# Optimization experiments

Hardware: AMD Instinct MI355X
Metric: run time of the kernel (lower is better)

The kernel has to match this reference:

```python
import jax, jax.numpy as jnp
import numpy as np

DIM = 96
D_STATE = 16
D_CONV = 3
D_INNER = 192   # int(DIM * 2.0)
DT_RANK = 6     # ceil(DIM / 16)
K = 4           # cross-scan directions
BATCH, H, W = 2, 56, 56


def setup_inputs() -> dict:
    key = jax.random.key(0)
    k = jax.random.split(key, 8)
    x = jax.random.normal(k[0], (BATCH, DIM, H, W), jnp.float32)
    W_in = jax.random.normal(k[1], (DIM, 2 * D_INNER), jnp.float32) / np.sqrt(DIM)
    W_conv = jax.random.normal(k[2], (D_INNER, 1, D_CONV, D_CONV), jnp.float32) / D_CONV
    b_conv = jnp.zeros((D_INNER,), jnp.float32)
    W_xproj = jax.random.normal(k[3], (K, D_INNER, DT_RANK + 2 * D_STATE), jnp.float32) / np.sqrt(D_INNER)
    W_dt = jax.random.normal(k[4], (K, DT_RANK, D_INNER), jnp.float32) / np.sqrt(DT_RANK)
    # dt bias init as in torch: dt ~ exp(U * (log 0.1 - log 0.001) + log 0.001), inv-softplus
    dt = jnp.exp(jax.random.uniform(k[5], (K, D_INNER), jnp.float32)
                 * (np.log(0.1) - np.log(0.001)) + np.log(0.001))
    dt = jnp.clip(dt, 1e-4, None)
    b_dt = dt + jnp.log(-jnp.expm1(-dt))
    A_logs = jnp.log(jnp.broadcast_to(jnp.arange(1, D_STATE + 1, dtype=jnp.float32),
                                      (K, D_INNER, D_STATE)))
    Ds = jnp.ones((K, D_INNER), jnp.float32)
    W_out = jax.random.normal(k[6], (D_INNER, DIM), jnp.float32) / np.sqrt(D_INNER)
    return dict(x=x, W_in=W_in, W_conv=W_conv, b_conv=b_conv, W_xproj=W_xproj,
                W_dt=W_dt, b_dt=b_dt, A_logs=A_logs, Ds=Ds, W_out=W_out)


def _ss2d(x, W_in, W_conv, b_conv, W_xproj, W_dt, b_dt, A_logs, Ds, W_out):
    Bsz, C, Hh, Ww = x.shape
    L = Hh * Ww
    # in_proj
    xf = x.transpose(0, 2, 3, 1).reshape(Bsz, L, C)        # (B, L, C)
    xz = xf @ W_in
    xp, z = jnp.split(xz, 2, axis=-1)                       # each (B, L, D)
    # depthwise conv + silu
    xi = xp.reshape(Bsz, Hh, Ww, -1).transpose(0, 3, 1, 2)  # (B, D, H, W)
    pad = D_CONV // 2
    xi = jax.lax.conv_general_dilated(
        xi, W_conv, (1, 1), ((pad, pad), (pad, pad)),
        feature_group_count=xi.shape[1],
        dimension_numbers=('NCHW', 'OIHW', 'NCHW')) + b_conv[None, :, None, None]
    xi = jax.nn.silu(xi)
    D = xi.shape[1]
    # cross-scan: 4 directions, each (B, L, D)
    x1 = xi.reshape(Bsz, D, L).transpose(0, 2, 1)
    x2 = xi[:, :, :, ::-1].reshape(Bsz, D, L).transpose(0, 2, 1)
    xt = xi.transpose(0, 1, 3, 2)                           # (B, D, W, H)
    x3 = xt.reshape(Bsz, D, L).transpose(0, 2, 1)
    x4 = xt[:, :, :, ::-1].reshape(Bsz, D, L).transpose(0, 2, 1)
    xs = jnp.stack([x1, x2, x3, x4])                        # (K, B, L, D)
    # per-direction projections, batched over K
    xdbl = jnp.einsum('kbld,kde->kble', xs, W_xproj)
    dr = xdbl[..., :DT_RANK]
    Bk = xdbl[..., DT_RANK:DT_RANK + D_STATE]               # (K, B, L, N)
    Ck = xdbl[..., DT_RANK + D_STATE:]                      # (K, B, L, N)
    delta = jax.nn.softplus(jnp.einsum('kblr,krd->kbld', dr, W_dt)
                            + b_dt[:, None, None, :])       # (K, B, L, D)
    A = -jnp.exp(A_logs)                                    # (K, D, N)

    def step(h, inp):
        x_i, d_i, B_i, C_i = inp  # (K,B,D), (K,B,D), (K,B,N), (K,B,N)
        dA = jnp.exp(d_i[..., None] * A[:, None])           # (K, B, D, N)
        h = dA * h + (d_i * x_i)[..., None] * B_i[:, :, None, :]
        y = jnp.einsum('kbdn,kbn->kbd', h, C_i)
        return h, y

    h0 = jnp.zeros((K, Bsz, D, D_STATE), xs.dtype)
    seq = (xs.transpose(2, 0, 1, 3), delta.transpose(2, 0, 1, 3),
           Bk.transpose(2, 0, 1, 3), Ck.transpose(2, 0, 1, 3))
    _, ys = jax.lax.scan(step, h0, seq)                     # (L, K, B, D)
    ys = ys.transpose(1, 2, 0, 3) + xs * Ds[:, None, None, :]  # (K, B, L, D)
    # cross-merge back to row-major (h w) order
    y1 = ys[0]
    y2 = ys[1].reshape(Bsz, Hh, Ww, D)[:, :, ::-1, :].reshape(Bsz, L, D)
    y3 = ys[2].reshape(Bsz, Ww, Hh, D).transpose(0, 2, 1, 3).reshape(Bsz, L, D)
    y4 = ys[3].reshape(Bsz, Ww, Hh, D)[:, :, ::-1, :].transpose(0, 2, 1, 3).reshape(Bsz, L, D)
    y = (y1 + y2 + y3 + y4) * jax.nn.silu(z)
    out = (y @ W_out).reshape(Bsz, Hh, Ww, C).transpose(0, 3, 1, 2)
    return out


def reference(x, W_in, W_conv, b_conv, W_xproj, W_dt, b_dt, A_logs, Ds, W_out):
    return _ss2d(x, W_in, W_conv, b_conv, W_xproj, W_dt, b_dt, A_logs, Ds, W_out)
```

## Files before the change

kernel.cpp:

```cpp
#include <hip/hip_runtime.h>
#include <math.h>

constexpr int BATCH  = 2;
constexpr int CDIM   = 96;
constexpr int HH     = 56;
constexpr int WW     = 56;
constexpr int LL     = HH * WW;
constexpr int DIN    = 192;
constexpr int NK     = 4;
constexpr int NST    = 16;
constexpr int RNK    = 6;
constexpr int EPROJ  = RNK + 2 * NST;
constexpr int SCH    = 64;
constexpr int NCH    = LL / SCH;
constexpr int CGRP   = DIN / 16;
constexpr int C_DPB  = 32;
constexpr int C_NBLK = DIN / C_DPB;

constexpr int STDU = SCH + 2;
constexpr int STB1 = SCH + 4;

constexpr size_t SZ_PX   = (size_t)BATCH * LL * DIN;
constexpr size_t OFF_XP  = 0;
constexpr size_t OFF_Z   = OFF_XP + SZ_PX;
constexpr size_t OFF_XI  = OFF_Z  + SZ_PX;
constexpr size_t OFF_DR  = OFF_XI + SZ_PX;
constexpr size_t SZ_DR   = (size_t)NK * BATCH * LL * 8;
constexpr size_t OFF_B   = OFF_DR + SZ_DR;
constexpr size_t SZ_BC   = (size_t)NK * BATCH * LL * NST;
constexpr size_t OFF_C   = OFF_B + SZ_BC;
constexpr size_t OFF_YD  = OFF_C + SZ_BC;
constexpr size_t SZ_YD   = (size_t)NK * BATCH * LL * DIN;
constexpr size_t OFF_HE  = OFF_YD + SZ_YD;
constexpr size_t SZ_HS   = (size_t)NK * BATCH * NCH * DIN * NST;
constexpr size_t OFF_WT  = OFF_HE + 2 * SZ_HS;
constexpr size_t SZ_WT   = (size_t)NK * EPROJ * DIN;

__device__ __forceinline__ float silu(float v) {
    return v / (1.0f + __expf(-v));
}

__device__ __forceinline__ float softplus_f(float x) {
    return (x > 20.0f) ? x : __logf(1.0f + __expf(x));
}

__device__ __forceinline__ int seq_to_lr(int k, int l) {
    int q = l / WW;
    int r = l - q * WW;
    if (k == 0) return l;
    if (k == 1) return q * WW + (WW - 1 - r);
    if (k == 2) return r * WW + q;
    return (WW - 1 - r) * WW + q;
}

__device__ __forceinline__ int spatial_to_seq(int k, int s) {
    int h = s / WW;
    int w = s - h * WW;
    if (k == 0) return s;
    if (k == 1) return h * WW + (WW - 1 - w);
    if (k == 2) return w * WW + h;
    return w * WW + (WW - 1 - h);
}

__device__ __forceinline__ size_t hs_idx(int c, int kb, int d, int n) {
    return ((size_t)(c * (NK * BATCH) + kb) * DIN + d) * NST + n;
}

__device__ __forceinline__ float4 delta4(
        float4 r03, float2 r45, const float4* wr, float4 bb4) {
    float4 raw = bb4;
    raw.x = fmaf(r03.x, wr[0].x, raw.x); raw.y = fmaf(r03.x, wr[0].y, raw.y);
    raw.z = fmaf(r03.x, wr[0].z, raw.z); raw.w = fmaf(r03.x, wr[0].w, raw.w);
    raw.x = fmaf(r03.y, wr[1].x, raw.x); raw.y = fmaf(r03.y, wr[1].y, raw.y);
    raw.z = fmaf(r03.y, wr[1].z, raw.z); raw.w = fmaf(r03.y, wr[1].w, raw.w);
    raw.x = fmaf(r03.z, wr[2].x, raw.x); raw.y = fmaf(r03.z, wr[2].y, raw.y);
    raw.z = fmaf(r03.z, wr[2].z, raw.z); raw.w = fmaf(r03.z, wr[2].w, raw.w);
    raw.x = fmaf(r03.w, wr[3].x, raw.x); raw.y = fmaf(r03.w, wr[3].y, raw.y);
    raw.z = fmaf(r03.w, wr[3].z, raw.z); raw.w = fmaf(r03.w, wr[3].w, raw.w);
    raw.x = fmaf(r45.x, wr[4].x, raw.x); raw.y = fmaf(r45.x, wr[4].y, raw.y);
    raw.z = fmaf(r45.x, wr[4].z, raw.z); raw.w = fmaf(r45.x, wr[4].w, raw.w);
    raw.x = fmaf(r45.y, wr[5].x, raw.x); raw.y = fmaf(r45.y, wr[5].y, raw.y);
    raw.z = fmaf(r45.y, wr[5].z, raw.z); raw.w = fmaf(r45.y, wr[5].w, raw.w);
    raw.x = softplus_f(raw.x); raw.y = softplus_f(raw.y);
    raw.z = softplus_f(raw.z); raw.w = softplus_f(raw.w);
    return raw;
}

constexpr int K1_PIX = 8;
__global__ __launch_bounds__(384) void k_inproj(
        const float* __restrict__ x, const float* __restrict__ W_in,
        const float* __restrict__ W_xproj,
        float* __restrict__ xp, float* __restrict__ z, float* __restrict__ Wt) {
    __shared__ float sxT[CDIM][K1_PIX];
    int gp0 = blockIdx.x * K1_PIX;
    int t   = threadIdx.x;
    int b   = gp0 / LL;
    int l0  = gp0 - b * LL;
    int gid = blockIdx.x * 384 + t;
    if (gid < NK * DIN * EPROJ) {
        int k = gid / (DIN * EPROJ);
        int r = gid % (DIN * EPROJ);
        int d = r / EPROJ;
        int e = r % EPROJ;
        Wt[((size_t)k * EPROJ + e) * DIN + d] = W_xproj[gid];
    }
    for (int i = t; i < CDIM * K1_PIX; i += 384) {
        int c = i >> 3, p = i & 7;
        sxT[c][p] = x[((size_t)(b * CDIM + c)) * LL + l0 + p];
    }
    __syncthreads();
    int e = t;
    float acc[K1_PIX];
#pragma unroll
    for (int p = 0; p < K1_PIX; p++) acc[p] = 0.0f;
    const float4* sx4 = (const float4*)sxT;
#pragma unroll 4
    for (int c = 0; c < CDIM; c++) {
        float w  = W_in[c * (2 * DIN) + e];
        float4 va = sx4[2 * c];
        float4 vb = sx4[2 * c + 1];
        acc[0] = fmaf(va.x, w, acc[0]); acc[1] = fmaf(va.y, w, acc[1]);
        acc[2] = fmaf(va.z, w, acc[2]); acc[3] = fmaf(va.w, w, acc[3]);
        acc[4] = fmaf(vb.x, w, acc[4]); acc[5] = fmaf(vb.y, w, acc[5]);
        acc[6] = fmaf(vb.z, w, acc[6]); acc[7] = fmaf(vb.w, w, acc[7]);
    }
    if (e < DIN) {
#pragma unroll
        for (int p = 0; p < K1_PIX; p++)
            xp[((size_t)(gp0 + p)) * DIN + e] = acc[p];
    } else {
        int e2 = e - DIN;
#pragma unroll
        for (int p = 0; p < K1_PIX; p++)
            z[((size_t)(gp0 + p)) * DIN + e2] = acc[p];
    }
}

constexpr int KC_PIX = 4;
__global__ __launch_bounds__(192) void k_conv(
        const float* __restrict__ xp, const float* __restrict__ Wc,
        const float* __restrict__ bc, float* __restrict__ xi) {
    __shared__ float sW[9][DIN];
    int t = threadIdx.x;
    for (int i = t; i < DIN * 9; i += 192) {
        int d = i / 9, tap = i % 9;
        sW[tap][d] = Wc[i];
    }
    __syncthreads();
    int p   = t / 48;
    int cg4 = (t % 48) * 4;
    int gp  = blockIdx.x * KC_PIX + p;
    int b   = gp / LL;
    int l   = gp - b * LL;
    int h   = l / WW;
    int w   = l - h * WW;
    float4 acc = *(const float4*)&bc[cg4];
#pragma unroll
    for (int dy = -1; dy <= 1; dy++) {
        int hh = h + dy;
        if (hh < 0 || hh >= HH) continue;
#pragma unroll
        for (int dx = -1; dx <= 1; dx++) {
            int ww = w + dx;
            if (ww < 0 || ww >= WW) continue;
            float4 xv = *(const float4*)&xp[((size_t)b * LL + hh * WW + ww) * DIN + cg4];
            float4 wv = *(const float4*)&sW[(dy + 1) * 3 + (dx + 1)][cg4];
            acc.x = fmaf(xv.x, wv.x, acc.x);
            acc.y = fmaf(xv.y, wv.y, acc.y);
            acc.z = fmaf(xv.z, wv.z, acc.z);
            acc.w = fmaf(xv.w, wv.w, acc.w);
        }
    }
    float4 o;
    o.x = silu(acc.x); o.y = silu(acc.y); o.z = silu(acc.z); o.w = silu(acc.w);
    *(float4*)&xi[(size_t)gp * DIN + cg4] = o;
}

constexpr int K3_PIX = 32;
__global__ __launch_bounds__(256) void k_xproj(
        const float* __restrict__ xi, const float* __restrict__ Wt,
        float* __restrict__ drbuf, float* __restrict__ Bbuf,
        float* __restrict__ Cbuf) {
    __shared__ float4 v4[K3_PIX][49];
    int k   = blockIdx.y;
    int gp0 = blockIdx.x * K3_PIX;
    int b   = gp0 / LL;
    int l0  = gp0 - b * LL;
    int t   = threadIdx.x;
    const float4* xin4 = (const float4*)(xi + (size_t)gp0 * DIN);
    for (int i = t; i < K3_PIX * 48; i += 256)
        v4[i / 48][i % 48] = xin4[i];
    const float4* wt4 = (const float4*)(Wt + (size_t)k * EPROJ * DIN);
    __syncthreads();
    int p0 = t & 15;
    int eg = t >> 4;
    bool has3 = (eg < EPROJ - 32);
    float acc[2][3] = {{0.f, 0.f, 0.f}, {0.f, 0.f, 0.f}};
#pragma unroll 4
    for (int j = 0; j < 48; j++) {
        float4 w0 = wt4[eg * 48 + j];
        float4 w1 = wt4[(eg + 16) * 48 + j];
        float4 w2 = has3 ? wt4[(eg + 32) * 48 + j] : make_float4(0.f, 0.f, 0.f, 0.f);
#pragma unroll
        for (int q = 0; q < 2; q++) {
            float4 vv = v4[p0 + 16 * q][j];
            acc[q][0] = fmaf(vv.x, w0.x, acc[q][0]); acc[q][0] = fmaf(vv.y, w0.y, acc[q][0]);
            acc[q][0] = fmaf(vv.z, w0.z, acc[q][0]); acc[q][0] = fmaf(vv.w, w0.w, acc[q][0]);
            acc[q][1] = fmaf(vv.x, w1.x, acc[q][1]); acc[q][1] = fmaf(vv.y, w1.y, acc[q][1]);
            acc[q][1] = fmaf(vv.z, w1.z, acc[q][1]); acc[q][1] = fmaf(vv.w, w1.w, acc[q][1]);
            acc[q][2] = fmaf(vv.x, w2.x, acc[q][2]); acc[q][2] = fmaf(vv.y, w2.y, acc[q][2]);
            acc[q][2] = fmaf(vv.z, w2.z, acc[q][2]); acc[q][2] = fmaf(vv.w, w2.w, acc[q][2]);
        }
    }
#pragma unroll
    for (int q = 0; q < 2; q++) {
        int p  = p0 + 16 * q;
        int ls = spatial_to_seq(k, l0 + p);
        size_t kb  = (size_t)(k * BATCH + b);
        size_t b8  = (kb * LL + ls) * 8;
        size_t b16 = (kb * LL + ls) * NST;
        if (eg < RNK) drbuf[b8 + eg] = acc[q][0];
        else          Bbuf[b16 + eg - RNK] = acc[q][0];
        int e1 = eg + 16;
        if (e1 < RNK + NST) Bbuf[b16 + e1 - RNK] = acc[q][1];
        else                Cbuf[b16 + e1 - RNK - NST] = acc[q][1];
        if (has3) Cbuf[b16 + eg + 32 - RNK - NST] = acc[q][2];
    }
}

__global__ __launch_bounds__(256) void k_scanA(
        const float* __restrict__ xi, const float* __restrict__ drbuf,
        const float* __restrict__ Bbuf, const float* __restrict__ A_logs,
        const float* __restrict__ W_dt, const float* __restrict__ b_dt,
        float2* __restrict__ sum2) {
    __shared__ float2 sDU2[16][STDU];
    __shared__ float  sB1t[16][STB1];
    __shared__ float  sT[16][68];
    int c   = blockIdx.x;
    int blk = blockIdx.y;
    int k   = blk / (BATCH * CGRP);
    int rem = blk % (BATCH * CGRP);
    int b   = rem / CGRP;
    int cg  = rem % CGRP;
    int d0  = cg * 16;
    int t    = threadIdx.x;
    int lane = t & 63, wave = t >> 6;
    int grp  = lane >> 4, n = lane & 15;
    int ch   = wave * 4 + grp;
    int d    = d0 + ch;
    float A = -__expf(A_logs[((size_t)(k * DIN + d)) * NST + n]);
    size_t kb = (size_t)(k * BATCH + b);
    const float* drp = drbuf + kb * LL * 8;
    const float* bp  = Bbuf  + kb * LL * NST;
    const float* up  = xi    + (size_t)b * LL * DIN;
    int ss  = t >> 2;
    int cc0 = (t & 3) * 4;
    float4 wr[RNK];
#pragma unroll
    for (int r = 0; r < RNK; r++)
        wr[r] = *(const float4*)(W_dt + ((size_t)k * RNK + r) * DIN + d0 + cc0);
    float4 bb4 = *(const float4*)(b_dt + k * DIN + d0 + cc0);
    int l0 = c * SCH;
    {
        int l  = l0 + ss;
        int lr = seq_to_lr(k, l);
        float4 r03 = *(const float4*)(drp + (size_t)l * 8);
        float2 r45 = *(const float2*)(drp + (size_t)l * 8 + 4);
        float4 dlt = delta4(r03, r45, wr, bb4);
        float4 u4  = *(const float4*)(up + (size_t)lr * DIN + d0 + cc0);
        float4 B4  = *(const float4*)(bp + (size_t)l * NST + cc0);
        sDU2[cc0 + 0][ss] = make_float2(dlt.x, dlt.x * u4.x);
        sDU2[cc0 + 1][ss] = make_float2(dlt.y, dlt.y * u4.y);
        sDU2[cc0 + 2][ss] = make_float2(dlt.z, dlt.z * u4.z);
        sDU2[cc0 + 3][ss] = make_float2(dlt.w, dlt.w * u4.w);
        sB1t[cc0 + 0][ss] = B4.x;
        sB1t[cc0 + 1][ss] = B4.y;
        sB1t[cc0 + 2][ss] = B4.z;
        sB1t[cc0 + 3][ss] = B4.w;
    }
    __syncthreads();
    if (t < 16) {
        float run = 0.0f;
#pragma unroll 8
        for (int j = SCH - 1; j >= 0; j--) {
            sT[t][j] = run;
            run += sDU2[t][j].x;
        }
        sT[t][SCH] = run;
    }
    __syncthreads();
    float h0 = 0.f, h1 = 0.f, h2 = 0.f, h3 = 0.f;
#pragma unroll 2
    for (int j = 0; j < SCH; j += 4) {
        float4 tq  = *(const float4*)&sT[ch][j];
        float4 duA = *(const float4*)&sDU2[ch][j];
        float4 duB = *(const float4*)&sDU2[ch][j + 2];
        float4 bq  = *(const float4*)&sB1t[n][j];
        h0 = fmaf(__expf(A * tq.x), duA.y * bq.x, h0);
        h1 = fmaf(__expf(A * tq.y), duA.w * bq.y, h1);
        h2 = fmaf(__expf(A * tq.z), duB.y * bq.z, h2);
        h3 = fmaf(__expf(A * tq.w), duB.w * bq.w, h3);
    }
    float h = (h0 + h1) + (h2 + h3);
    float P = __expf(A * sT[ch][SCH]);
    sum2[hs_idx(c, (int)kb, d, n)] = make_float2(P, h);
}

__global__ __launch_bounds__(128) void k_scanC(
        const float* __restrict__ xi, const float* __restrict__ drbuf,
        const float* __restrict__ Bbuf, const float* __restrict__ Cbuf,
        const float* __restrict__ A_logs, const float* __restrict__ W_dt,
        const float* __restrict__ b_dt,
        const float2* __restrict__ sum2,
        float* __restrict__ ydir) {
    __shared__ float2 sDU2[C_DPB][65];
    __shared__ float4 sB4[SCH][5];
    __shared__ float4 sC4[SCH][5];
    __shared__ float  sY[C_DPB][65];
    int c   = blockIdx.x;
    int blk = blockIdx.y;
    int k   = blk / (BATCH * C_NBLK);
    int rem = blk % (BATCH * C_NBLK);
    int b   = rem / C_NBLK;
    int g   = rem % C_NBLK;
    int d0  = g * C_DPB;
    int t    = threadIdx.x;
    int lane = t & 63, wave = t >> 6;
    int dl   = wave * 16 + (lane >> 2);
    int ng   = lane & 3;
    int n0   = ng * 4;
    int d    = d0 + dl;
    size_t kb = (size_t)(k * BATCH + b);
    const float* drp = drbuf + kb * LL * 8;
    const float* bp  = Bbuf  + kb * LL * NST;
    const float* cp  = Cbuf  + kb * LL * NST;
    const float* up  = xi    + (size_t)b * LL * DIN;
    float*       yp  = ydir  + kb * LL * DIN;
    float4 al = *(const float4*)(A_logs + ((size_t)(k * DIN + d)) * NST + n0);
    float A0 = -__expf(al.x), A1 = -__expf(al.y);
    float A2 = -__expf(al.z), A3 = -__expf(al.w);
    float h0 = 0.f, h1 = 0.f, h2 = 0.f, h3 = 0.f;
    {
        int j = 0;
        for (; j + 4 <= c; j += 4) {
            const float4* p0 = (const float4*)(sum2 + hs_idx(j + 0, (int)kb, d, n0));
            const float4* p1 = (const float4*)(sum2 + hs_idx(j + 1, (int)kb, d, n0));
            const float4* p2 = (const float4*)(sum2 + hs_idx(j + 2, (int)kb, d, n0));
            const float4* p3 = (const float4*)(sum2 + hs_idx(j + 3, (int)kb, d, n0));
            float4 a0 = p0[0], b0 = p0[1];
            float4 a1 = p1[0], b1 = p1[1];
            float4 a2 = p2[0], b2 = p2[1];
            float4 a3 = p3[0], b3 = p3[1];
            h0 = fmaf(a0.x, h0, a0.y); h1 = fmaf(a0.z, h1, a0.w);
            h2 = fmaf(b0.x, h2, b0.y); h3 = fmaf(b0.z, h3, b0.w);
            h0 = fmaf(a1.x, h0, a1.y); h1 = fmaf(a1.z, h1, a1.w);
            h2 = fmaf(b1.x, h2, b1.y); h3 = fmaf(b1.z, h3, b1.w);
            h0 = fmaf(a2.x, h0, a2.y); h1 = fmaf(a2.z, h1, a2.w);
            h2 = fmaf(b2.x, h2, b2.y); h3 = fmaf(b2.z, h3, b2.w);
            h0 = fmaf(a3.x, h0, a3.y); h1 = fmaf(a3.z, h1, a3.w);
            h2 = fmaf(b3.x, h2, b3.y); h3 = fmaf(b3.z, h3, b3.w);
        }
        for (; j < c; j++) {
            const float4* pj = (const float4*)(sum2 + hs_idx(j, (int)kb, d, n0));
            float4 a = pj[0], bq = pj[1];
            h0 = fmaf(a.x, h0, a.y); h1 = fmaf(a.z, h1, a.w);
            h2 = fmaf(bq.x, h2, bq.y); h3 = fmaf(bq.z, h3, bq.w);
        }
    }
    int l0 = c * SCH;
    {
        int ss = t & 63;
        int dg = t >> 6;
        int l  = l0 + ss;
        int lr = seq_to_lr(k, l);
        float4 r03 = *(const float4*)(drp + (size_t)l * 8);
        float2 r45 = *(const float2*)(drp + (size_t)l * 8 + 4);
#pragma unroll
        for (int q = 0; q < 4; q++) {
            int cc0 = dg * 16 + q * 4;
            float4 wr[RNK];
#pragma unroll
            for (int r = 0; r < RNK; r++)
                wr[r] = *(const float4*)(W_dt + ((size_t)k * RNK + r) * DIN + d0 + cc0);
            float4 bb4 = *(const float4*)(b_dt + k * DIN + d0 + cc0);
            float4 dlt = delta4(r03, r45, wr, bb4);
            float4 u4  = *(const float4*)(up + (size_t)lr * DIN + d0 + cc0);
            sDU2[cc0 + 0][ss] = make_float2(dlt.x, dlt.x * u4.x);
            sDU2[cc0 + 1][ss] = make_float2(dlt.y, dlt.y * u4.y);
            sDU2[cc0 + 2][ss] = make_float2(dlt.z, dlt.z * u4.z);
            sDU2[cc0 + 3][ss] = make_float2(dlt.w, dlt.w * u4.w);
        }
        int s2 = t & 63;
        int l2 = l0 + s2;
        if (t < 64) {
#pragma unroll
            for (int q = 0; q < 4; q++)
                sB4[s2][q] = *(const float4*)(bp + (size_t)l2 * NST + q * 4);
        } else {
#pragma unroll
            for (int q = 0; q < 4; q++)
                sC4[s2][q] = *(const float4*)(cp + (size_t)l2 * NST + q * 4);
        }
    }
    __syncthreads();
#pragma unroll 4
    for (int s = 0; s < SCH; s++) {
        float2 du = sDU2[dl][s];
        float4 B4 = sB4[s][ng];
        float4 C4 = sC4[s][ng];
        h0 = fmaf(__expf(du.x * A0), h0, du.y * B4.x);
        h1 = fmaf(__expf(du.x * A1), h1, du.y * B4.y);
        h2 = fmaf(__expf(du.x * A2), h2, du.y * B4.z);
        h3 = fmaf(__expf(du.x * A3), h3, du.y * B4.w);
        float yq = (h0 * C4.x + h1 * C4.y) + (h2 * C4.z + h3 * C4.w);
        yq += __int_as_float(__builtin_amdgcn_update_dpp(
                0, __float_as_int(yq), 0xB1, 0xf, 0xf, true));
        yq += __int_as_float(__builtin_amdgcn_update_dpp(
                0, __float_as_int(yq), 0x4E, 0xf, 0xf, true));
        if (ng == 0) sY[dl][s] = yq;
    }
    __syncthreads();
    for (int i = t; i < SCH * (C_DPB / 4); i += 128) {
        int dq = i & (C_DPB / 4 - 1);
        int s  = i >> 3;
        int lr = seq_to_lr(k, l0 + s);
        float4 v = make_float4(sY[dq * 4 + 0][s], sY[dq * 4 + 1][s],
                               sY[dq * 4 + 2][s], sY[dq * 4 + 3][s]);
        *(float4*)&yp[(size_t)lr * DIN + d0 + dq * 4] = v;
    }
}

constexpr int K5_PIX = 8;
__global__ __launch_bounds__(192) void k_out(
        const float* __restrict__ ydir, const float* __restrict__ xi,
        const float* __restrict__ zbuf, const float* __restrict__ Ds,
        const float* __restrict__ W_out, float* __restrict__ out) {
    __shared__ float g[DIN][12];
    __shared__ float so[CDIM][9];
    int gp0 = blockIdx.x * K5_PIX;
    int b   = gp0 / LL;
    int l0  = gp0 - b * LL;
    int t   = threadIdx.x;
    for (int i = t; i < K5_PIX * DIN; i += 192) {
        int p = i / DIN, dd = i % DIN;
        size_t off = (size_t)(gp0 + p) * DIN + dd;
        float y = ydir[off] + ydir[SZ_PX + off]
                + ydir[2 * SZ_PX + off] + ydir[3 * SZ_PX + off];
        float dsum = Ds[dd] + Ds[DIN + dd] + Ds[2 * DIN + dd] + Ds[3 * DIN + dd];
        y = fmaf(xi[off], dsum, y);
        g[dd][p] = y * silu(zbuf[off]);
    }
    __syncthreads();
    int f    = t % CDIM;
    int half = t / CDIM;
    float acc[4] = {0.f, 0.f, 0.f, 0.f};
#pragma unroll 4
    for (int dd = 0; dd < DIN; dd++) {
        float wv = W_out[dd * CDIM + f];
        float4 gv = *(const float4*)&g[dd][half * 4];
        acc[0] = fmaf(gv.x, wv, acc[0]);
        acc[1] = fmaf(gv.y, wv, acc[1]);
        acc[2] = fmaf(gv.z, wv, acc[2]);
        acc[3] = fmaf(gv.w, wv, acc[3]);
    }
#pragma unroll
    for (int p = 0; p < 4; p++) so[f][half * 4 + p] = acc[p];
    __syncthreads();
    for (int i = t; i < CDIM * K5_PIX; i += 192) {
        int f2 = i / K5_PIX, p2 = i % K5_PIX;
        out[((size_t)(b * CDIM + f2)) * LL + l0 + p2] = so[f2][p2];
    }
}

extern "C" void kernel_launch(void* const* d_in, const int* in_sizes, int n_in,
                              void* d_out, int out_size, void* d_ws, size_t ws_size,
                              hipStream_t stream) {
    const float* x       = (const float*)d_in[0];
    const float* W_in    = (const float*)d_in[1];
    const float* W_conv  = (const float*)d_in[2];
    const float* b_conv  = (const float*)d_in[3];
    const float* W_xproj = (const float*)d_in[4];
    const float* W_dt    = (const float*)d_in[5];
    const float* b_dt    = (const float*)d_in[6];
    const float* A_logs  = (const float*)d_in[7];
    const float* Ds      = (const float*)d_in[8];
    const float* W_out   = (const float*)d_in[9];
    float* out = (float*)d_out;
    float* ws  = (float*)d_ws;

    float* xp    = ws + OFF_XP;
    float* z     = ws + OFF_Z;
    float* xi    = ws + OFF_XI;
    float* drbuf = ws + OFF_DR;
    float* Bbuf  = ws + OFF_B;
    float* Cbuf  = ws + OFF_C;
    float* ydir  = ws + OFF_YD;
    float2* sum2 = (float2*)(ws + OFF_HE);
    float* Wt    = ws + OFF_WT;

    k_inproj<<<(BATCH * LL) / K1_PIX, 384, 0, stream>>>(x, W_in, W_xproj, xp, z, Wt);
    k_conv<<<(BATCH * LL) / KC_PIX, 192, 0, stream>>>(xp, W_conv, b_conv, xi);
    dim3 g3((BATCH * LL) / K3_PIX, NK);
    k_xproj<<<g3, 256, 0, stream>>>(xi, Wt, drbuf, Bbuf, Cbuf);
    dim3 gsA(NCH, NK * BATCH * CGRP);
    k_scanA<<<gsA, 256, 0, stream>>>(xi, drbuf, Bbuf, A_logs, W_dt, b_dt, sum2);
    dim3 gsC(NCH, NK * BATCH * C_NBLK);
    k_scanC<<<gsC, 128, 0, stream>>>(xi, drbuf, Bbuf, Cbuf, A_logs, W_dt, b_dt, sum2, ydir);
    k_out<<<(BATCH * LL) / K5_PIX, 192, 0, stream>>>(ydir, xi, z, Ds, W_out, out);
}
```

Before: 206.0 us.

## Use sequential recurrence in scanA, widen scanC blocks, store y directly

In scanA, the reverse prefix sum over delta and its extra barrier are replaced by a sequential recurrence that tracks both h and the running decay product P. scanC now handles 64 channels per block with 256 threads. It also drops the shared-memory y staging buffer and second barrier, writing each y value straight to global memory through a cached lr index. The sequential scan adds a dependency chain. The direct writes are scalar stores with a stride of DIN floats instead of coalesced float4 stores.

```diff
diff --git a/kernel.cpp b/kernel.cpp
--- a/kernel.cpp
+++ b/kernel.cpp
@@ -14,7 +14,7 @@
 constexpr int SCH    = 64;
 constexpr int NCH    = LL / SCH;
 constexpr int CGRP   = DIN / 16;
-constexpr int C_DPB  = 32;
+constexpr int C_DPB  = 64;
 constexpr int C_NBLK = DIN / C_DPB;
 
 constexpr int STDU = SCH + 2;
@@ -235,7 +235,6 @@
         float2* __restrict__ sum2) {
     __shared__ float2 sDU2[16][STDU];
     __shared__ float  sB1t[16][STB1];
-    __shared__ float  sT[16][68];
     int c   = blockIdx.x;
     int blk = blockIdx.y;
     int k   = blk / (BATCH * CGRP);
@@ -279,34 +278,22 @@
         sB1t[cc0 + 3][ss] = B4.w;
     }
     __syncthreads();
-    if (t < 16) {
-        float run = 0.0f;
-#pragma unroll 8
-        for (int j = SCH - 1; j >= 0; j--) {
-            sT[t][j] = run;
-            run += sDU2[t][j].x;
-        }
-        sT[t][SCH] = run;
-    }
-    __syncthreads();
-    float h0 = 0.f, h1 = 0.f, h2 = 0.f, h3 = 0.f;
+    float h = 0.0f, P = 1.0f;
 #pragma unroll 2
-    for (int j = 0; j < SCH; j += 4) {
-        float4 tq  = *(const float4*)&sT[ch][j];
-        float4 duA = *(const float4*)&sDU2[ch][j];
-        float4 duB = *(const float4*)&sDU2[ch][j + 2];
-        float4 bq  = *(const float4*)&sB1t[n][j];
-        h0 = fmaf(__expf(A * tq.x), duA.y * bq.x, h0);
-        h1 = fmaf(__expf(A * tq.y), duA.w * bq.y, h1);
-        h2 = fmaf(__expf(A * tq.z), duB.y * bq.z, h2);
-        h3 = fmaf(__expf(A * tq.w), duB.w * bq.w, h3);
-    }
-    float h = (h0 + h1) + (h2 + h3);
-    float P = __expf(A * sT[ch][SCH]);
+    for (int s4 = 0; s4 < SCH; s4 += 4) {
+        float4 duA = *(const float4*)&sDU2[ch][s4];
+        float4 duB = *(const float4*)&sDU2[ch][s4 + 2];
+        float4 bq  = *(const float4*)&sB1t[n][s4];
+        float dA;
+        dA = __expf(duA.x * A); h = fmaf(dA, h, duA.y * bq.x); P *= dA;
+        dA = __expf(duA.z * A); h = fmaf(dA, h, duA.w * bq.y); P *= dA;
+        dA = __expf(duB.x * A); h = fmaf(dA, h, duB.y * bq.z); P *= dA;
+        dA = __expf(duB.z * A); h = fmaf(dA, h, duB.w * bq.w); P *= dA;
+    }
     sum2[hs_idx(c, (int)kb, d, n)] = make_float2(P, h);
 }
 
-__global__ __launch_bounds__(128) void k_scanC(
+__global__ __launch_bounds__(256) void k_scanC(
         const float* __restrict__ xi, const float* __restrict__ drbuf,
         const float* __restrict__ Bbuf, const float* __restrict__ Cbuf,
         const float* __restrict__ A_logs, const float* __restrict__ W_dt,
@@ -316,7 +303,7 @@
     __shared__ float2 sDU2[C_DPB][65];
     __shared__ float4 sB4[SCH][5];
     __shared__ float4 sC4[SCH][5];
-    __shared__ float  sY[C_DPB][65];
+    __shared__ int    sLR[SCH];
     int c   = blockIdx.x;
     int blk = blockIdx.y;
     int k   = blk / (BATCH * C_NBLK);
@@ -373,6 +360,7 @@
         int dg = t >> 6;
         int l  = l0 + ss;
         int lr = seq_to_lr(k, l);
+        if (t < 64) sLR[ss] = lr;
         float4 r03 = *(const float4*)(drp + (size_t)l * 8);
         float2 r45 = *(const float2*)(drp + (size_t)l * 8 + 4);
 #pragma unroll
@@ -390,19 +378,18 @@
             sDU2[cc0 + 2][ss] = make_float2(dlt.z, dlt.z * u4.z);
             sDU2[cc0 + 3][ss] = make_float2(dlt.w, dlt.w * u4.w);
         }
-        int s2 = t & 63;
-        int l2 = l0 + s2;
-        if (t < 64) {
+        if (dg == 0) {
 #pragma unroll
             for (int q = 0; q < 4; q++)
-                sB4[s2][q] = *(const float4*)(bp + (size_t)l2 * NST + q * 4);
-        } else {
+                sB4[ss][q] = *(const float4*)(bp + (size_t)l * NST + q * 4);
+        } else if (dg == 1) {
 #pragma unroll
             for (int q = 0; q < 4; q++)
-                sC4[s2][q] = *(const float4*)(cp + (size_t)l2 * NST + q * 4);
-        }
-    }
-    __syncthreads();
+                sC4[ss][q] = *(const float4*)(cp + (size_t)l * NST + q * 4);
+        }
+    }
+    __syncthreads();
+    int dglob = d;
 #pragma unroll 4
     for (int s = 0; s < SCH; s++) {
         float2 du = sDU2[dl][s];
@@ -417,16 +404,8 @@
                 0, __float_as_int(yq), 0xB1, 0xf, 0xf, true));
         yq += __int_as_float(__builtin_amdgcn_update_dpp(
                 0, __float_as_int(yq), 0x4E, 0xf, 0xf, true));
-        if (ng == 0) sY[dl][s] = yq;
-    }
-    __syncthreads();
-    for (int i = t; i < SCH * (C_DPB / 4); i += 128) {
-        int dq = i & (C_DPB / 4 - 1);
-        int s  = i >> 3;
-        int lr = seq_to_lr(k, l0 + s);
-        float4 v = make_float4(sY[dq * 4 + 0][s], sY[dq * 4 + 1][s],
-                               sY[dq * 4 + 2][s], sY[dq * 4 + 3][s]);
-        *(float4*)&yp[(size_t)lr * DIN + d0 + dq * 4] = v;
+        if (ng == 0)
+            yp[(size_t)sLR[s] * DIN + dglob] = yq;
     }
 }
 
@@ -505,6 +484,6 @@
     dim3 gsA(NCH, NK * BATCH * CGRP);
     k_scanA<<<gsA, 256, 0, stream>>>(xi, drbuf, Bbuf, A_logs, W_dt, b_dt, sum2);
     dim3 gsC(NCH, NK * BATCH * C_NBLK);
-    k_scanC<<<gsC, 128, 0, stream>>>(xi, drbuf, Bbuf, Cbuf, A_logs, W_dt, b_dt, sum2, ydir);
+    k_scanC<<<gsC, 256, 0, stream>>>(xi, drbuf, Bbuf, Cbuf, A_logs, W_dt, b_dt, sum2, ydir);
     k_out<<<(BATCH * LL) / K5_PIX, 192, 0, stream>>>(ydir, xi, z, Ds, W_out, out);
 }
```

Measured after the change: 204.1 us. Within noise of the previous version (-1.0%).
